# Kernel tuning notes

Hardware: AMD Instinct MI355X
Metric: run time of the kernel (lower is better)

The kernel has to match this reference:

```python
import jax, jax.numpy as jnp
import numpy as np

N_NODES = 100000
N_EDGES = 1600000
IN_DIM = 128
HID = 256
OUT_DIM = 1
NUM_GRAPHS = 2048


def setup_inputs() -> dict:
    key = jax.random.key(0)
    ks = jax.random.split(key, 12)
    x = jax.random.normal(ks[0], (N_NODES, IN_DIM), dtype=jnp.float32)
    edge_index = jax.random.randint(ks[1], (2, N_EDGES), 0, N_NODES, dtype=jnp.int32)
    batch = jnp.sort(jax.random.randint(ks[2], (N_NODES,), 0, NUM_GRAPHS, dtype=jnp.int32))
    def glorot(k, shape):
        lim = float(np.sqrt(6.0 / (shape[0] + shape[1])))
        return jax.random.uniform(k, shape, jnp.float32, -lim, lim)
    W1 = glorot(ks[3], (IN_DIM, HID));  b1 = jnp.zeros((HID,), jnp.float32)
    W2 = glorot(ks[4], (HID, HID));     b2 = jnp.zeros((HID,), jnp.float32)
    Wf1 = glorot(ks[5], (HID, HID // 2)); bf1 = jnp.zeros((HID // 2,), jnp.float32)
    Wf2 = glorot(ks[6], (HID // 2, OUT_DIM)); bf2 = jnp.zeros((OUT_DIM,), jnp.float32)
    return {"x": x, "edge_index": edge_index, "batch": batch,
            "W1": W1, "b1": b1, "W2": W2, "b2": b2,
            "Wf1": Wf1, "bf1": bf1, "Wf2": Wf2, "bf2": bf2}


def _gcn_conv(x, W, b, src, dst, norm, num_nodes):
    # PyG GCNConv: h = X W; out[dst] += norm_e * h[src]; out += b
    h = x @ W                                   # [N, F]
    msg = h[src] * norm[:, None]                # [E', F] gather + scale
    agg = jax.ops.segment_sum(msg, dst, num_segments=num_nodes)
    return agg + b


def reference(x, edge_index, batch, W1, b1, W2, b2, Wf1, bf1, Wf2, bf2):
    n = x.shape[0]
    loop = jnp.arange(n, dtype=edge_index.dtype)
    src = jnp.concatenate([edge_index[0], loop])  # add self-loops (GCN default)
    dst = jnp.concatenate([edge_index[1], loop])
    # symmetric normalization: deg over A+I at dst index
    deg = jax.ops.segment_sum(jnp.ones_like(src, dtype=x.dtype), dst, num_segments=n)
    dinv = jnp.where(deg > 0, jax.lax.rsqrt(deg), 0.0)
    norm = dinv[src] * dinv[dst]                 # [E']

    h = jax.nn.relu(_gcn_conv(x, W1, b1, src, dst, norm, n))
    h = jax.nn.relu(_gcn_conv(h, W2, b2, src, dst, norm, n))

    # global_mean_pool over graphs
    sums = jax.ops.segment_sum(h, batch, num_segments=NUM_GRAPHS)
    cnts = jax.ops.segment_sum(jnp.ones((n,), h.dtype), batch, num_segments=NUM_GRAPHS)
    pooled = sums / jnp.maximum(cnts, 1.0)[:, None]   # [G, HID]

    out = jax.nn.relu(pooled @ Wf1 + bf1) @ Wf2 + bf2  # [G, OUT_DIM]
    return out
```

## Files before the change

kernel.cpp:

```cpp
#include <hip/hip_runtime.h>
#include <hip/hip_bf16.h>

#define N_NODES 100000
#define N_EDGES 1600000
#define IN_DIM 128
#define HID 256
#define NUM_GRAPHS 2048
#define M_PAD 100096
#define SCAN_BLOCKS 98

typedef __bf16 bf16x8 __attribute__((ext_vector_type(8)));
typedef float f32x4 __attribute__((ext_vector_type(4)));

__device__ inline unsigned short f2bf(float x) {
    union { __hip_bfloat16 h; unsigned short u; } v;
    v.h = __float2bfloat16(x);
    return v.u;
}
__device__ inline float bf2f(unsigned short u) {
    return __uint_as_float(((unsigned int)u) << 16);
}
__device__ inline int rfl(int x) { return __builtin_amdgcn_readfirstlane(x); }

__global__ void count_deg_kernel(const int* __restrict__ ei, int* __restrict__ deg,
                                 int* __restrict__ eord) {
    int e = blockIdx.x * blockDim.x + threadIdx.x;
    if (e < N_EDGES) {
        eord[e] = atomicAdd(&deg[ei[N_EDGES + e]], 1);
    }
}

__global__ __launch_bounds__(1024) void blocksum_kernel(const int* __restrict__ deg,
                                                        int* __restrict__ bsum,
                                                        float* __restrict__ dinv) {
    int i = blockIdx.x * 1024 + threadIdx.x;
    int v = (i < N_NODES) ? deg[i] : 0;
    if (i < N_NODES) dinv[i] = rsqrtf((float)(v + 1));
    __shared__ int s[1024];
    int t = threadIdx.x;
    s[t] = v;
    __syncthreads();
#pragma unroll
    for (int off = 512; off > 0; off >>= 1) {
        if (t < off) s[t] += s[t + off];
        __syncthreads();
    }
    if (t == 0) bsum[blockIdx.x] = s[0];
}

__global__ __launch_bounds__(128) void bscan_kernel(int* __restrict__ bsum) {
    __shared__ int s[128];
    int t = threadIdx.x;
    int v = (t < SCAN_BLOCKS) ? bsum[t] : 0;
    s[t] = v;
    __syncthreads();
#pragma unroll
    for (int off = 1; off < 128; off <<= 1) {
        int x = (t >= off) ? s[t - off] : 0;
        __syncthreads();
        s[t] += x;
        __syncthreads();
    }
    if (t < SCAN_BLOCKS) bsum[t] = (t > 0) ? s[t - 1] : 0;
}

__global__ __launch_bounds__(1024) void scanout_kernel(const int* __restrict__ deg,
                                                       const int* __restrict__ bsum,
                                                       int* __restrict__ rowptr) {
    int i = blockIdx.x * 1024 + threadIdx.x;
    int t = threadIdx.x;
    int v = (i < N_NODES) ? deg[i] : 0;
    __shared__ int s[1024];
    s[t] = v;
    __syncthreads();
#pragma unroll
    for (int off = 1; off < 1024; off <<= 1) {
        int x = (t >= off) ? s[t - off] : 0;
        __syncthreads();
        s[t] += x;
        __syncthreads();
    }
    int base = bsum[blockIdx.x];
    int excl = (t > 0) ? s[t - 1] : 0;
    if (i < N_NODES) rowptr[i] = base + excl;
    if (i == N_NODES - 1) rowptr[N_NODES] = base + s[t];
}

__global__ void fill_kernel(const int* __restrict__ ei, const int* __restrict__ rowptr,
                            const int* __restrict__ eord, int* __restrict__ esrc) {
    int e = blockIdx.x * blockDim.x + threadIdx.x;
    if (e < N_EDGES) {
        int dst = ei[N_EDGES + e];
        esrc[rowptr[dst] + eord[e]] = ei[e];
    }
}

__global__ void x2bf_kernel(const float* __restrict__ x, unsigned short* __restrict__ xb) {
    size_t i = ((size_t)blockIdx.x * 256 + threadIdx.x) * 4;
    float4 v = *(const float4*)(x + i);
    ushort4 o;
    o.x = f2bf(v.x); o.y = f2bf(v.y); o.z = f2bf(v.z); o.w = f2bf(v.w);
    *(ushort4*)(xb + i) = o;
}

__global__ void wsplit_all_kernel(const float* __restrict__ W1, const float* __restrict__ W2,
                                  unsigned short* __restrict__ W1th, unsigned short* __restrict__ W1tl,
                                  unsigned short* __restrict__ W2th, unsigned short* __restrict__ W2tl) {
    int idx = blockIdx.x * 256 + threadIdx.x;
    if (idx < IN_DIM * 256) {
        int k = idx >> 8, n = idx & 255;
        float w = W1[idx];
        unsigned short h = f2bf(w);
        unsigned short l = f2bf(w - bf2f(h));
        W1th[n * IN_DIM + k] = h;
        W1tl[n * IN_DIM + k] = l;
    } else {
        int i2 = idx - IN_DIM * 256;
        int k = i2 >> 8, n = i2 & 255;
        float w = W2[i2];
        unsigned short h = f2bf(w);
        unsigned short l = f2bf(w - bf2f(h));
        W2th[n * HID + k] = h;
        W2tl[n * HID + k] = l;
    }
}

__global__ __launch_bounds__(256) void agg128_kernel(const unsigned short* __restrict__ X,
                                                     const int* __restrict__ esrc,
                                                     const int* __restrict__ rowptr,
                                                     const float* __restrict__ dinv,
                                                     unsigned short* __restrict__ Ah,
                                                     unsigned short* __restrict__ Al) {
    int node = rfl(blockIdx.x * 4 + (threadIdx.x >> 6));
    int lane = threadIdx.x & 63;
    float ddst = dinv[node];
    int s = rfl(rowptr[node]);
    int e = rfl(rowptr[node + 1]);

    float w0 = ddst * ddst;
    ushort2 h0 = *((const ushort2*)(X + (size_t)node * 128) + lane);
    float2 acc = make_float2(w0 * bf2f(h0.x), w0 * bf2f(h0.y));

    int j = s;
    for (; j + 8 <= e; j += 8) {
        int si[8];
#pragma unroll
        for (int u = 0; u < 8; u++) si[u] = rfl(esrc[j + u]);
        ushort2 xv[8];
#pragma unroll
        for (int u = 0; u < 8; u++)
            xv[u] = *((const ushort2*)(X + (size_t)si[u] * 128) + lane);
        float a[8];
#pragma unroll
        for (int u = 0; u < 8; u++) a[u] = dinv[si[u]] * ddst;
#pragma unroll
        for (int u = 0; u < 8; u++) {
            acc.x = fmaf(a[u], bf2f(xv[u].x), acc.x);
            acc.y = fmaf(a[u], bf2f(xv[u].y), acc.y);
        }
    }
    for (; j + 4 <= e; j += 4) {
        int si[4];
#pragma unroll
        for (int u = 0; u < 4; u++) si[u] = rfl(esrc[j + u]);
        ushort2 xv[4];
#pragma unroll
        for (int u = 0; u < 4; u++)
            xv[u] = *((const ushort2*)(X + (size_t)si[u] * 128) + lane);
        float a[4];
#pragma unroll
        for (int u = 0; u < 4; u++) a[u] = dinv[si[u]] * ddst;
#pragma unroll
        for (int u = 0; u < 4; u++) {
            acc.x = fmaf(a[u], bf2f(xv[u].x), acc.x);
            acc.y = fmaf(a[u], bf2f(xv[u].y), acc.y);
        }
    }
    for (; j < e; j++) {
        int src = rfl(esrc[j]);
        float w = dinv[src] * ddst;
        ushort2 xv = *((const ushort2*)(X + (size_t)src * 128) + lane);
        acc.x = fmaf(w, bf2f(xv.x), acc.x);
        acc.y = fmaf(w, bf2f(xv.y), acc.y);
    }
    size_t o = (size_t)node * 128 + lane * 2;
    ushort2 hi, lo;
    hi.x = f2bf(acc.x); lo.x = f2bf(acc.x - bf2f(hi.x));
    hi.y = f2bf(acc.y); lo.y = f2bf(acc.y - bf2f(hi.y));
    *(ushort2*)(Ah + o) = hi;
    *(ushort2*)(Al + o) = lo;
}

__global__ __launch_bounds__(256) void agg256_kernel(const unsigned short* __restrict__ H,
                                                     const int* __restrict__ esrc,
                                                     const int* __restrict__ rowptr,
                                                     const float* __restrict__ dinv,
                                                     unsigned short* __restrict__ Ah) {
    int node = rfl(blockIdx.x * 4 + (threadIdx.x >> 6));
    int lane = threadIdx.x & 63;
    float ddst = dinv[node];
    int s = rfl(rowptr[node]);
    int e = rfl(rowptr[node + 1]);

    float w0 = ddst * ddst;
    ushort4 h0 = *((const ushort4*)(H + (size_t)node * 256) + lane);
    float4 acc = make_float4(w0 * bf2f(h0.x), w0 * bf2f(h0.y),
                             w0 * bf2f(h0.z), w0 * bf2f(h0.w));

    int j = s;
    for (; j + 8 <= e; j += 8) {
        int si[8];
#pragma unroll
        for (int u = 0; u < 8; u++) si[u] = rfl(esrc[j + u]);
        ushort4 xv[8];
#pragma unroll
        for (int u = 0; u < 8; u++)
            xv[u] = *((const ushort4*)(H + (size_t)si[u] * 256) + lane);
        float a[8];
#pragma unroll
        for (int u = 0; u < 8; u++) a[u] = dinv[si[u]] * ddst;
#pragma unroll
        for (int u = 0; u < 8; u++) {
            acc.x = fmaf(a[u], bf2f(xv[u].x), acc.x);
            acc.y = fmaf(a[u], bf2f(xv[u].y), acc.y);
            acc.z = fmaf(a[u], bf2f(xv[u].z), acc.z);
            acc.w = fmaf(a[u], bf2f(xv[u].w), acc.w);
        }
    }
    for (; j + 4 <= e; j += 4) {
        int si[4];
#pragma unroll
        for (int u = 0; u < 4; u++) si[u] = rfl(esrc[j + u]);
        ushort4 xv[4];
#pragma unroll
        for (int u = 0; u < 4; u++)
            xv[u] = *((const ushort4*)(H + (size_t)si[u] * 256) + lane);
        float a[4];
#pragma unroll
        for (int u = 0; u < 4; u++) a[u] = dinv[si[u]] * ddst;
#pragma unroll
        for (int u = 0; u < 4; u++) {
            acc.x = fmaf(a[u], bf2f(xv[u].x), acc.x);
            acc.y = fmaf(a[u], bf2f(xv[u].y), acc.y);
            acc.z = fmaf(a[u], bf2f(xv[u].z), acc.z);
            acc.w = fmaf(a[u], bf2f(xv[u].w), acc.w);
        }
    }
    for (; j < e; j++) {
        int src = rfl(esrc[j]);
        float w = dinv[src] * ddst;
        ushort4 xv = *((const ushort4*)(H + (size_t)src * 256) + lane);
        acc.x = fmaf(w, bf2f(xv.x), acc.x);
        acc.y = fmaf(w, bf2f(xv.y), acc.y);
        acc.z = fmaf(w, bf2f(xv.z), acc.z);
        acc.w = fmaf(w, bf2f(xv.w), acc.w);
    }
    size_t o = (size_t)node * 256 + lane * 4;
    ushort4 hi;
    hi.x = f2bf(acc.x); hi.y = f2bf(acc.y);
    hi.z = f2bf(acc.z); hi.w = f2bf(acc.w);
    *(ushort4*)(Ah + o) = hi;
}

template <int K, bool ASPLIT>
__launch_bounds__(256, 2)
__global__ void mfma_gemm_bias_relu(const unsigned short* __restrict__ Ah,
                                    const unsigned short* __restrict__ Al,
                                    const unsigned short* __restrict__ Bh,
                                    const unsigned short* __restrict__ Bl,
                                    const float* __restrict__ bias,
                                    unsigned short* __restrict__ Cout) {
    constexpr int NT = ASPLIT ? 4 : 3;
    __shared__ __align__(16) unsigned short lds[NT * 128 * 32];
    unsigned short* Ahs = lds;
    unsigned short* Als = lds + 4096;
    unsigned short* Bhs = lds + (ASPLIT ? 8192 : 4096);
    unsigned short* Bls = lds + (ASPLIT ? 12288 : 8192);

    int tid = threadIdx.x;
    int bm = blockIdx.x * 128;
    int bn = blockIdx.y * 128;
    int wid = tid >> 6, lane = tid & 63;
    int wm = wid & 1, wn = wid >> 1;
    int lrow = lane & 15, quad = lane >> 4;

    f32x4 acc[4][4];
#pragma unroll
    for (int mi = 0; mi < 4; mi++)
#pragma unroll
        for (int ni = 0; ni < 4; ni++) acc[mi][ni] = (f32x4){0.f, 0.f, 0.f, 0.f};

    for (int k0 = 0; k0 < K; k0 += 32) {
#pragma unroll
        for (int i = 0; i < NT * 2; i++) {
            int c = tid + 256 * i;
            int tile = c >> 9;
            int w = c & 511;
            int row = w >> 2;
            int part = w & 3;
            const unsigned short* g;
            if (ASPLIT) {
                if (tile == 0)      g = Ah + (size_t)(bm + row) * K + k0 + part * 8;
                else if (tile == 1) g = Al + (size_t)(bm + row) * K + k0 + part * 8;
                else if (tile == 2) g = Bh + (size_t)(bn + row) * K + k0 + part * 8;
                else                g = Bl + (size_t)(bn + row) * K + k0 + part * 8;
            } else {
                if (tile == 0)      g = Ah + (size_t)(bm + row) * K + k0 + part * 8;
                else if (tile == 1) g = Bh + (size_t)(bn + row) * K + k0 + part * 8;
                else                g = Bl + (size_t)(bn + row) * K + k0 + part * 8;
            }
            ulonglong2 v = *(const ulonglong2*)g;
            *(ulonglong2*)&lds[(tile << 12) + row * 32 + part * 8] = v;
        }
        __syncthreads();

        bf16x8 ah[4], al[4], bh[4], bl[4];
#pragma unroll
        for (int mi = 0; mi < 4; mi++) {
            int r = wm * 64 + mi * 16 + lrow;
            ah[mi] = *(const bf16x8*)&Ahs[r * 32 + quad * 8];
            if (ASPLIT) al[mi] = *(const bf16x8*)&Als[r * 32 + quad * 8];
        }
#pragma unroll
        for (int ni = 0; ni < 4; ni++) {
            int r = wn * 64 + ni * 16 + lrow;
            bh[ni] = *(const bf16x8*)&Bhs[r * 32 + quad * 8];
            bl[ni] = *(const bf16x8*)&Bls[r * 32 + quad * 8];
        }
#pragma unroll
        for (int mi = 0; mi < 4; mi++)
#pragma unroll
            for (int ni = 0; ni < 4; ni++) {
                acc[mi][ni] = __builtin_amdgcn_mfma_f32_16x16x32_bf16(ah[mi], bh[ni], acc[mi][ni], 0, 0, 0);
                acc[mi][ni] = __builtin_amdgcn_mfma_f32_16x16x32_bf16(ah[mi], bl[ni], acc[mi][ni], 0, 0, 0);
                if (ASPLIT)
                    acc[mi][ni] = __builtin_amdgcn_mfma_f32_16x16x32_bf16(al[mi], bh[ni], acc[mi][ni], 0, 0, 0);
            }
        __syncthreads();
    }

    float bv[4];
#pragma unroll
    for (int ni = 0; ni < 4; ni++) bv[ni] = bias[bn + wn * 64 + ni * 16 + lrow];
#pragma unroll
    for (int mi = 0; mi < 4; mi++) {
        int row0 = bm + wm * 64 + mi * 16 + quad * 4;
#pragma unroll
        for (int ni = 0; ni < 4; ni++) {
            int col = bn + wn * 64 + ni * 16 + lrow;
#pragma unroll
            for (int r = 0; r < 4; r++) {
                int row = row0 + r;
                if (row < N_NODES) {
                    float v = fmaxf(acc[mi][ni][r] + bv[ni], 0.f);
                    Cout[(size_t)row * 256 + col] = f2bf(v);
                }
            }
        }
    }
}

__global__ __launch_bounds__(256) void pool_mlp_kernel(const unsigned short* __restrict__ h,
                                                       const int* __restrict__ batch,
                                                       const float* __restrict__ Wf1,
                                                       const float* __restrict__ bf1,
                                                       const float* __restrict__ Wf2,
                                                       const float* __restrict__ bf2,
                                                       float* __restrict__ out) {
    int g = blockIdx.x;
    int t = threadIdx.x;
    __shared__ int bounds[2];
    if (t < 2) {
        int target = g + t;
        int lo = 0, hi = N_NODES;
        while (lo < hi) {
            int mid = (lo + hi) >> 1;
            if (batch[mid] < target) lo = mid + 1;
            else hi = mid;
        }
        bounds[t] = lo;
    }
    __syncthreads();
    int lo = bounds[0], hi = bounds[1];

    float acc = 0.f;
    for (int n = lo; n < hi; n++) acc += bf2f(h[(size_t)n * HID + t]);
    float inv = (hi > lo) ? 1.0f / (float)(hi - lo) : 0.f;
    __shared__ float p[256];
    p[t] = acc * inv;
    __syncthreads();

    float hv = 0.f;
    if (t < 128) {
        float a = bf1[t];
#pragma unroll 8
        for (int k = 0; k < 256; k++) a = fmaf(p[k], Wf1[k * 128 + t], a);
        hv = fmaxf(a, 0.f) * Wf2[t];
    }
#pragma unroll
    for (int off = 32; off > 0; off >>= 1) hv += __shfl_down(hv, off, 64);
    __shared__ float partial[4];
    if ((t & 63) == 0) partial[t >> 6] = hv;
    __syncthreads();
    if (t == 0) out[g] = partial[0] + partial[1] + bf2[0];
}

extern "C" void kernel_launch(void* const* d_in, const int* in_sizes, int n_in,
                              void* d_out, int out_size, void* d_ws, size_t ws_size,
                              hipStream_t stream) {
    const float* x   = (const float*)d_in[0];
    const int*   ei  = (const int*)d_in[1];
    const int*   bat = (const int*)d_in[2];
    const float* W1  = (const float*)d_in[3];
    const float* b1  = (const float*)d_in[4];
    const float* W2  = (const float*)d_in[5];
    const float* b2  = (const float*)d_in[6];
    const float* Wf1 = (const float*)d_in[7];
    const float* bf1 = (const float*)d_in[8];
    const float* Wf2 = (const float*)d_in[9];
    const float* bf2 = (const float*)d_in[10];
    float* out = (float*)d_out;

    char* ws = (char*)d_ws;
    int*   deg    = (int*)(ws);
    float* dinv   = (float*)(ws + 0x0080000);
    int*   rowptr = (int*)(ws + 0x0100000);
    int*   bsum   = (int*)(ws + 0x01F0000);
    int*   esrc   = (int*)(ws + 0x0200000);
    unsigned short* W1th = (unsigned short*)(ws + 0x0820000);
    unsigned short* W1tl = (unsigned short*)(ws + 0x0830000);
    unsigned short* W2th = (unsigned short*)(ws + 0x0840000);
    unsigned short* W2tl = (unsigned short*)(ws + 0x0860000);
    unsigned short* A1h  = (unsigned short*)(ws + 0x0880000);
    int*   eord   = (int*)(ws + 0x20F0000);
    unsigned short* A1l  = (unsigned short*)(ws + 0x20F0000);
    unsigned short* A2   = (unsigned short*)(ws + 0x0880000);
    unsigned short* xbf  = (unsigned short*)(ws + 0x6A40000);
    unsigned short* H1bf = (unsigned short*)(ws + 0x6A40000);
    unsigned short* H2bf = (unsigned short*)(ws + 0x6A40000);
    (void)ws_size;

    hipMemsetAsync(deg, 0, (size_t)N_NODES * sizeof(int), stream);

    x2bf_kernel<<<(N_NODES * IN_DIM / 4) / 256, 256, 0, stream>>>(x, xbf);
    wsplit_all_kernel<<<((IN_DIM + HID) * 256) / 256, 256, 0, stream>>>(W1, W2, W1th, W1tl, W2th, W2tl);

    count_deg_kernel<<<(N_EDGES + 255) / 256, 256, 0, stream>>>(ei, deg, eord);
    blocksum_kernel<<<SCAN_BLOCKS, 1024, 0, stream>>>(deg, bsum, dinv);
    bscan_kernel<<<1, 128, 0, stream>>>(bsum);
    scanout_kernel<<<SCAN_BLOCKS, 1024, 0, stream>>>(deg, bsum, rowptr);
    fill_kernel<<<(N_EDGES + 255) / 256, 256, 0, stream>>>(ei, rowptr, eord, esrc);

    agg128_kernel<<<N_NODES / 4, 256, 0, stream>>>(xbf, esrc, rowptr, dinv, A1h, A1l);
    {
        dim3 grid(M_PAD / 128, 2);
        mfma_gemm_bias_relu<IN_DIM, true><<<grid, 256, 0, stream>>>(A1h, A1l, W1th, W1tl, b1, H1bf);
    }

    agg256_kernel<<<N_NODES / 4, 256, 0, stream>>>(H1bf, esrc, rowptr, dinv, A2);
    {
        dim3 grid(M_PAD / 128, 2);
        mfma_gemm_bias_relu<HID, false><<<grid, 256, 0, stream>>>(A2, nullptr, W2th, W2tl, b2, H2bf);
    }

    pool_mlp_kernel<<<NUM_GRAPHS, 256, 0, stream>>>(H2bf, bat, Wf1, bf1, Wf2, bf2, out);
}
```

Measured before the change: 545.5 us.

## Fold symmetric GCN normalization into producer kernels to drop per-edge dinv gathers

The source-side normalization dinv[src] is pre-applied to node features: x is scaled during the bf16 conversion, and H1 is scaled in the first GEMM epilogue. The aggregation kernels then do plain sums and multiply once by dinv[dst], which removes the random dinv gather and multiply on every edge. Aggregation outputs are also written with nontemporal stores. The x conversion now has to wait for the degree computation, and the scaling happens before bf16 rounding, which slightly changes numerics.

```diff
diff --git a/kernel.cpp b/kernel.cpp
--- a/kernel.cpp
+++ b/kernel.cpp
@@ -95,11 +95,15 @@
     }
 }
 
-__global__ void x2bf_kernel(const float* __restrict__ x, unsigned short* __restrict__ xb) {
+__global__ void x2bf_kernel(const float* __restrict__ x, const float* __restrict__ dinv,
+                            unsigned short* __restrict__ xb) {
     size_t i = ((size_t)blockIdx.x * 256 + threadIdx.x) * 4;
+    int node = (int)(i >> 7);
+    float dv = dinv[node];
     float4 v = *(const float4*)(x + i);
     ushort4 o;
-    o.x = f2bf(v.x); o.y = f2bf(v.y); o.z = f2bf(v.z); o.w = f2bf(v.w);
+    o.x = f2bf(v.x * dv); o.y = f2bf(v.y * dv);
+    o.z = f2bf(v.z * dv); o.w = f2bf(v.w * dv);
     *(ushort4*)(xb + i) = o;
 }
 
@@ -137,9 +141,8 @@
     int s = rfl(rowptr[node]);
     int e = rfl(rowptr[node + 1]);
 
-    float w0 = ddst * ddst;
     ushort2 h0 = *((const ushort2*)(X + (size_t)node * 128) + lane);
-    float2 acc = make_float2(w0 * bf2f(h0.x), w0 * bf2f(h0.y));
+    float2 acc = make_float2(bf2f(h0.x), bf2f(h0.y));
 
     int j = s;
     for (; j + 8 <= e; j += 8) {
@@ -150,13 +153,10 @@
 #pragma unroll
         for (int u = 0; u < 8; u++)
             xv[u] = *((const ushort2*)(X + (size_t)si[u] * 128) + lane);
-        float a[8];
-#pragma unroll
-        for (int u = 0; u < 8; u++) a[u] = dinv[si[u]] * ddst;
 #pragma unroll
         for (int u = 0; u < 8; u++) {
-            acc.x = fmaf(a[u], bf2f(xv[u].x), acc.x);
-            acc.y = fmaf(a[u], bf2f(xv[u].y), acc.y);
+            acc.x += bf2f(xv[u].x);
+            acc.y += bf2f(xv[u].y);
         }
     }
     for (; j + 4 <= e; j += 4) {
@@ -167,28 +167,27 @@
 #pragma unroll
         for (int u = 0; u < 4; u++)
             xv[u] = *((const ushort2*)(X + (size_t)si[u] * 128) + lane);
-        float a[4];
-#pragma unroll
-        for (int u = 0; u < 4; u++) a[u] = dinv[si[u]] * ddst;
 #pragma unroll
         for (int u = 0; u < 4; u++) {
-            acc.x = fmaf(a[u], bf2f(xv[u].x), acc.x);
-            acc.y = fmaf(a[u], bf2f(xv[u].y), acc.y);
+            acc.x += bf2f(xv[u].x);
+            acc.y += bf2f(xv[u].y);
         }
     }
     for (; j < e; j++) {
         int src = rfl(esrc[j]);
-        float w = dinv[src] * ddst;
         ushort2 xv = *((const ushort2*)(X + (size_t)src * 128) + lane);
-        acc.x = fmaf(w, bf2f(xv.x), acc.x);
-        acc.y = fmaf(w, bf2f(xv.y), acc.y);
-    }
+        acc.x += bf2f(xv.x);
+        acc.y += bf2f(xv.y);
+    }
+    acc.x *= ddst;
+    acc.y *= ddst;
     size_t o = (size_t)node * 128 + lane * 2;
-    ushort2 hi, lo;
-    hi.x = f2bf(acc.x); lo.x = f2bf(acc.x - bf2f(hi.x));
-    hi.y = f2bf(acc.y); lo.y = f2bf(acc.y - bf2f(hi.y));
-    *(ushort2*)(Ah + o) = hi;
-    *(ushort2*)(Al + o) = lo;
+    unsigned short hx = f2bf(acc.x), hy = f2bf(acc.y);
+    unsigned short lx = f2bf(acc.x - bf2f(hx)), ly = f2bf(acc.y - bf2f(hy));
+    __builtin_nontemporal_store((unsigned int)hx | ((unsigned int)hy << 16),
+                                (unsigned int*)(Ah + o));
+    __builtin_nontemporal_store((unsigned int)lx | ((unsigned int)ly << 16),
+                                (unsigned int*)(Al + o));
 }
 
 __global__ __launch_bounds__(256) void agg256_kernel(const unsigned short* __restrict__ H,
@@ -202,10 +201,8 @@
     int s = rfl(rowptr[node]);
     int e = rfl(rowptr[node + 1]);
 
-    float w0 = ddst * ddst;
     ushort4 h0 = *((const ushort4*)(H + (size_t)node * 256) + lane);
-    float4 acc = make_float4(w0 * bf2f(h0.x), w0 * bf2f(h0.y),
-                             w0 * bf2f(h0.z), w0 * bf2f(h0.w));
+    float4 acc = make_float4(bf2f(h0.x), bf2f(h0.y), bf2f(h0.z), bf2f(h0.w));
 
     int j = s;
     for (; j + 8 <= e; j += 8) {
@@ -216,15 +213,12 @@
 #pragma unroll
         for (int u = 0; u < 8; u++)
             xv[u] = *((const ushort4*)(H + (size_t)si[u] * 256) + lane);
-        float a[8];
-#pragma unroll
-        for (int u = 0; u < 8; u++) a[u] = dinv[si[u]] * ddst;
 #pragma unroll
         for (int u = 0; u < 8; u++) {
-            acc.x = fmaf(a[u], bf2f(xv[u].x), acc.x);
-            acc.y = fmaf(a[u], bf2f(xv[u].y), acc.y);
-            acc.z = fmaf(a[u], bf2f(xv[u].z), acc.z);
-            acc.w = fmaf(a[u], bf2f(xv[u].w), acc.w);
+            acc.x += bf2f(xv[u].x);
+            acc.y += bf2f(xv[u].y);
+            acc.z += bf2f(xv[u].z);
+            acc.w += bf2f(xv[u].w);
         }
     }
     for (; j + 4 <= e; j += 4) {
@@ -235,40 +229,40 @@
 #pragma unroll
         for (int u = 0; u < 4; u++)
             xv[u] = *((const ushort4*)(H + (size_t)si[u] * 256) + lane);
-        float a[4];
-#pragma unroll
-        for (int u = 0; u < 4; u++) a[u] = dinv[si[u]] * ddst;
 #pragma unroll
         for (int u = 0; u < 4; u++) {
-            acc.x = fmaf(a[u], bf2f(xv[u].x), acc.x);
-            acc.y = fmaf(a[u], bf2f(xv[u].y), acc.y);
-            acc.z = fmaf(a[u], bf2f(xv[u].z), acc.z);
-            acc.w = fmaf(a[u], bf2f(xv[u].w), acc.w);
+            acc.x += bf2f(xv[u].x);
+            acc.y += bf2f(xv[u].y);
+            acc.z += bf2f(xv[u].z);
+            acc.w += bf2f(xv[u].w);
         }
     }
     for (; j < e; j++) {
         int src = rfl(esrc[j]);
-        float w = dinv[src] * ddst;
         ushort4 xv = *((const ushort4*)(H + (size_t)src * 256) + lane);
-        acc.x = fmaf(w, bf2f(xv.x), acc.x);
-        acc.y = fmaf(w, bf2f(xv.y), acc.y);
-        acc.z = fmaf(w, bf2f(xv.z), acc.z);
-        acc.w = fmaf(w, bf2f(xv.w), acc.w);
-    }
+        acc.x += bf2f(xv.x);
+        acc.y += bf2f(xv.y);
+        acc.z += bf2f(xv.z);
+        acc.w += bf2f(xv.w);
+    }
+    acc.x *= ddst; acc.y *= ddst; acc.z *= ddst; acc.w *= ddst;
     size_t o = (size_t)node * 256 + lane * 4;
-    ushort4 hi;
-    hi.x = f2bf(acc.x); hi.y = f2bf(acc.y);
-    hi.z = f2bf(acc.z); hi.w = f2bf(acc.w);
-    *(ushort4*)(Ah + o) = hi;
-}
-
-template <int K, bool ASPLIT>
+    unsigned long long v =
+        (unsigned long long)f2bf(acc.x) |
+        ((unsigned long long)f2bf(acc.y) << 16) |
+        ((unsigned long long)f2bf(acc.z) << 32) |
+        ((unsigned long long)f2bf(acc.w) << 48);
+    __builtin_nontemporal_store(v, (unsigned long long*)(Ah + o));
+}
+
+template <int K, bool ASPLIT, bool SCALEOUT>
 __launch_bounds__(256, 2)
 __global__ void mfma_gemm_bias_relu(const unsigned short* __restrict__ Ah,
                                     const unsigned short* __restrict__ Al,
                                     const unsigned short* __restrict__ Bh,
                                     const unsigned short* __restrict__ Bl,
                                     const float* __restrict__ bias,
+                                    const float* __restrict__ dscale,
                                     unsigned short* __restrict__ Cout) {
     constexpr int NT = ASPLIT ? 4 : 3;
     __shared__ __align__(16) unsigned short lds[NT * 128 * 32];
@@ -345,6 +339,12 @@
 #pragma unroll
     for (int mi = 0; mi < 4; mi++) {
         int row0 = bm + wm * 64 + mi * 16 + quad * 4;
+        float dsc[4];
+        if (SCALEOUT) {
+#pragma unroll
+            for (int r = 0; r < 4; r++)
+                dsc[r] = (row0 + r < N_NODES) ? dscale[row0 + r] : 0.f;
+        }
 #pragma unroll
         for (int ni = 0; ni < 4; ni++) {
             int col = bn + wn * 64 + ni * 16 + lrow;
@@ -353,6 +353,7 @@
                 int row = row0 + r;
                 if (row < N_NODES) {
                     float v = fmaxf(acc[mi][ni][r] + bv[ni], 0.f);
+                    if (SCALEOUT) v *= dsc[r];
                     Cout[(size_t)row * 256 + col] = f2bf(v);
                 }
             }
@@ -442,11 +443,12 @@
 
     hipMemsetAsync(deg, 0, (size_t)N_NODES * sizeof(int), stream);
 
-    x2bf_kernel<<<(N_NODES * IN_DIM / 4) / 256, 256, 0, stream>>>(x, xbf);
-    wsplit_all_kernel<<<((IN_DIM + HID) * 256) / 256, 256, 0, stream>>>(W1, W2, W1th, W1tl, W2th, W2tl);
-
     count_deg_kernel<<<(N_EDGES + 255) / 256, 256, 0, stream>>>(ei, deg, eord);
     blocksum_kernel<<<SCAN_BLOCKS, 1024, 0, stream>>>(deg, bsum, dinv);
+
+    x2bf_kernel<<<(N_NODES * IN_DIM / 4) / 256, 256, 0, stream>>>(x, dinv, xbf);
+    wsplit_all_kernel<<<((IN_DIM + HID) * 256) / 256, 256, 0, stream>>>(W1, W2, W1th, W1tl, W2th, W2tl);
+
     bscan_kernel<<<1, 128, 0, stream>>>(bsum);
     scanout_kernel<<<SCAN_BLOCKS, 1024, 0, stream>>>(deg, bsum, rowptr);
     fill_kernel<<<(N_EDGES + 255) / 256, 256, 0, stream>>>(ei, rowptr, eord, esrc);
@@ -454,13 +456,13 @@
     agg128_kernel<<<N_NODES / 4, 256, 0, stream>>>(xbf, esrc, rowptr, dinv, A1h, A1l);
     {
         dim3 grid(M_PAD / 128, 2);
-        mfma_gemm_bias_relu<IN_DIM, true><<<grid, 256, 0, stream>>>(A1h, A1l, W1th, W1tl, b1, H1bf);
+        mfma_gemm_bias_relu<IN_DIM, true, true><<<grid, 256, 0, stream>>>(A1h, A1l, W1th, W1tl, b1, dinv, H1bf);
     }
 
     agg256_kernel<<<N_NODES / 4, 256, 0, stream>>>(H1bf, esrc, rowptr, dinv, A2);
     {
         dim3 grid(M_PAD / 128, 2);
-        mfma_gemm_bias_relu<HID, false><<<grid, 256, 0, stream>>>(A2, nullptr, W2th, W2tl, b2, H2bf);
+        mfma_gemm_bias_relu<HID, false, false><<<grid, 256, 0, stream>>>(A2, nullptr, W2th, W2tl, b2, nullptr, H2bf);
     }
 
     pool_mlp_kernel<<<NUM_GRAPHS, 256, 0, stream>>>(H2bf, bat, Wf1, bf1, Wf2, bf2, out);
```

Measured after the change: 551.8 us. Within noise of the previous version (+1.2%).
